# Kernel tuning notes

Hardware: AMD Instinct MI355X
Metric: run time of the kernel (lower is better)

Reference implementation:

```python
import jax, jax.numpy as jnp
import numpy as np

B, T, H, K = 128, 32, 256, 32


def setup_inputs() -> dict:
    key = jax.random.key(0)
    ks = jax.random.split(key, 24)
    s = 0.02  # small weight scale keeps exp(pdf) stable

    def n(k, shape, scale=s):
        return jax.random.normal(k, shape, dtype=jnp.float32) * scale

    inp = {
        "input_encoded": jax.random.normal(ks[0], (B, T, H), dtype=jnp.float32),
        "y_prev": jax.random.normal(ks[1], (B, T), dtype=jnp.float32),
        "attn_W1": n(ks[2], (H, 3 * H)),
        "attn_b1": n(ks[3], (H,)),
        "attn_W2": n(ks[4], (1, H)),
        "attn_b2": n(ks[5], (1,)),
        "fc_W": n(ks[6], (1, H + 1)),
        "fc_b": n(ks[7], (1,)),
        "var_W": n(ks[8], (H, H + 1)),
        "var_b": n(ks[9], (H,)),
        "W_ih": n(ks[10], (4 * H, 1)),
        "W_hh": n(ks[11], (4 * H, H)),
        "b_ih": n(ks[12], (4 * H,)),
        "b_hh": n(ks[13], (4 * H,)),
        "fc_dec_W": n(ks[14], (1, H)),
        "fc_dec_b": n(ks[15], (1,)),
        "pdf_W": n(ks[16], (1, H + 1)),
        "pdf_b": n(ks[17], (1,)),
        "fc_enc_W": n(ks[18], (1, H)),
        "fc_enc_b": n(ks[19], (1,)),
        "num_particles": K,
    }
    return inp


def reference(input_encoded, y_prev, attn_W1, attn_b1, attn_W2, attn_b2,
              fc_W, fc_b, var_W, var_b, W_ih, W_hh, b_ih, b_hh,
              fc_dec_W, fc_dec_b, pdf_W, pdf_b, fc_enc_W, fc_enc_b,
              num_particles):
    Bn, Tn, Hn = input_encoded.shape
    Kn = num_particles
    base = jax.random.key(42)
    arB = jnp.arange(Bn)

    def step(carry, xs):
        hiddens, cells = carry  # each (K*B, H), flat index = k*B + b
        t, y_t = xs  # y_t: (B,)
        k1, k2 = jax.random.split(jax.random.fold_in(base, t))
        # particle means (torch: mean over dim 0 of (K, B, H) view)
        hm = hiddens.reshape(Kn, Bn, Hn).mean(axis=0)  # (B, H)
        cm = cells.reshape(Kn, Bn, Hn).mean(axis=0)
        # attention over encoder timesteps
        x = jnp.concatenate([
            jnp.broadcast_to(hm[:, None, :], (Bn, Tn, Hn)),
            jnp.broadcast_to(cm[:, None, :], (Bn, Tn, Hn)),
            input_encoded], axis=2)  # (B, T, 3H)
        a = jnp.tanh(x @ attn_W1.T + attn_b1) @ attn_W2.T + attn_b2  # (B, T, 1)
        beta = jax.nn.softmax(a[..., 0], axis=1)  # (B, T)
        context = jnp.einsum('bt,bth->bh', beta, input_encoded)  # (B, H)
        y_tilde = jnp.concatenate([context, y_t[:, None]], axis=1) @ fc_W.T + fc_b  # (B, 1)
        var = jnp.concatenate([y_tilde, hm], axis=1) @ var_W.T + var_b  # (B, H)
        # single-step LSTM cell over all particles (torch gate order i,f,g,o)
        x_in = jnp.tile(y_tilde, (Kn, 1))  # (K*B, 1)
        gates = x_in @ W_ih.T + b_ih + hiddens @ W_hh.T + b_hh  # (K*B, 4H)
        i, f, g, o = jnp.split(gates, 4, axis=1)
        c_new = jax.nn.sigmoid(f) * cells + jax.nn.sigmoid(i) * jnp.tanh(g)
        h_new = jax.nn.sigmoid(o) * jnp.tanh(c_new)
        # reparameterization: h = mu + eps * softplus(var)
        std = jnp.tile(jax.nn.softplus(var), (Kn, 1))  # (K*B, H)
        eps = jax.random.normal(k1, (Kn * Bn, Hn), dtype=h_new.dtype)
        h_new = h_new + eps * std
        # sort_hidden: per-batch argsort of 1-d projection, gather hiddens only
        proj = h_new @ fc_dec_W.T + fc_dec_b  # (K*B, 1)
        idx = jnp.argsort(proj.reshape(Kn, Bn).T, axis=1)  # (B, K)
        flat = (arB[:, None] + idx * Bn).T.reshape(-1)  # (K*B,)
        h_sorted = h_new[flat]
        # particle weights (replicates torch's view(-1, K, 1) reshape exactly)
        y = jnp.concatenate([h_sorted, jnp.tile(y_tilde, (Kn, 1))], axis=1)
        prob = jnp.exp(y @ pdf_W.T + pdf_b).reshape(Bn, Kn, 1)
        prob = prob / prob.sum(axis=1, keepdims=True)
        # soft-resampling: multinomial over (B, K) rows (torch: prob.view(K,-1).T)
        logits = jnp.log(prob.reshape(Kn, Bn).T)  # (B, K)
        samp = jax.random.categorical(k2, logits, shape=(Kn, Bn))  # (K, B)
        flat2 = (samp * Bn + arB[None, :]).reshape(-1)
        return (h_sorted[flat2], c_new[flat2]), context

    h0 = jnp.zeros((Kn * Bn, Hn), dtype=input_encoded.dtype)
    (hiddens, _), contexts = jax.lax.scan(step, (h0, h0), (jnp.arange(Tn), y_prev.T))
    context = contexts[-1]
    hm = hiddens.reshape(Kn, Bn, Hn).mean(axis=0)  # (B, H)
    y_pred = hm @ fc_dec_W.T + fc_dec_b + context @ fc_enc_W.T + fc_enc_b  # (B, 1)
    return y_pred
```

## Files before the change

kernel.cpp:

```cpp
#include <hip/hip_runtime.h>
#include <cstdint>


#define Bn 128
#define Tn 32
#define Hn 256
#define Kn 32

__host__ __device__ inline void tf2x32(uint32_t k0, uint32_t k1, uint32_t x0, uint32_t x1,
                                       uint32_t &o0, uint32_t &o1) {
  uint32_t ks2 = k0 ^ k1 ^ 0x1BD11BDAu;
  x0 += k0; x1 += k1;
#define TFR(r) { x0 += x1; x1 = (x1 << r) | (x1 >> (32 - r)); x1 ^= x0; }
  TFR(13) TFR(15) TFR(26) TFR(6)
  x0 += k1;  x1 += ks2 + 1u;
  TFR(17) TFR(29) TFR(16) TFR(24)
  x0 += ks2; x1 += k0 + 2u;
  TFR(13) TFR(15) TFR(26) TFR(6)
  x0 += k0;  x1 += k1 + 3u;
  TFR(17) TFR(29) TFR(16) TFR(24)
  x0 += k1;  x1 += ks2 + 4u;
  TFR(13) TFR(15) TFR(26) TFR(6)
  x0 += ks2; x1 += k0 + 5u;
#undef TFR
  o0 = x0; o1 = x1;
}

__device__ __forceinline__ float erfinv_xla(float x) {
  float w = -log1pf(-x * x);
  float p;
  if (w < 5.0f) {
    w = w - 2.5f;
    p = 2.81022636e-08f;
    p = fmaf(p, w, 3.43273939e-07f);
    p = fmaf(p, w, -3.5233877e-06f);
    p = fmaf(p, w, -4.39150654e-06f);
    p = fmaf(p, w, 0.00021858087f);
    p = fmaf(p, w, -0.00125372503f);
    p = fmaf(p, w, -0.00417768164f);
    p = fmaf(p, w, 0.246640727f);
    p = fmaf(p, w, 1.50140941f);
  } else {
    w = sqrtf(w) - 3.0f;
    p = -0.000200214257f;
    p = fmaf(p, w, 0.000100950558f);
    p = fmaf(p, w, 0.00134934322f);
    p = fmaf(p, w, -0.00367342844f);
    p = fmaf(p, w, 0.00573950773f);
    p = fmaf(p, w, -0.0076224613f);
    p = fmaf(p, w, 0.00943887047f);
    p = fmaf(p, w, 1.00167406f);
    p = fmaf(p, w, 2.83297682f);
  }
  return p * x;
}

__device__ __forceinline__ float sigmoid_xla(float x) {
  return 0.5f + 0.5f * tanhf(0.5f * x);
}

__device__ __forceinline__ float u01_from_bits(uint32_t bits) {
  return __uint_as_float((bits >> 9) | 0x3F800000u) - 1.0f;
}

__device__ __forceinline__ float normal_from_idx(uint32_t ka, uint32_t kb, uint32_t idx) {
  uint32_t o0, o1; tf2x32(ka, kb, 0u, idx, o0, o1);
  float f = u01_from_bits(o0 ^ o1);
  const float LO = __uint_as_float(0xBF7FFFFFu);
  float u = fmaxf(LO, f * 2.0f + LO);
  return __uint_as_float(0x3FB504F3u) * erfinv_xla(u);
}

__device__ __forceinline__ float gumbel_from_idx(uint32_t ka, uint32_t kb, uint32_t idx) {
  uint32_t o0, o1; tf2x32(ka, kb, 0u, idx, o0, o1);
  float f = u01_from_bits(o0 ^ o1);
  const float TINY = __uint_as_float(0x00800000u);
  float u = fmaxf(TINY, f + TINY);
  return -logf(-logf(u));
}


__global__ void darnn_p0(const float* __restrict__ W1, const float* __restrict__ Whh,
                         const float* __restrict__ varW,
                         float* __restrict__ W1hT, float* __restrict__ W1cT,
                         float* __restrict__ W1eT, float* __restrict__ WhhT,
                         float* __restrict__ varWT) {
  int bid = blockIdx.x, tid = threadIdx.x;
  if (bid < 768) {
    int part = bid >> 8, j = bid & 255;
    float v = W1[tid * 768 + part * 256 + j];
    float* dst = (part == 0) ? W1hT : (part == 1) ? W1cT : W1eT;
    dst[j * 256 + tid] = v;
  } else if (bid < 1024) {
    int j = bid - 768;
    for (int idx = tid; idx < 1024; idx += 256) {
      int h = idx >> 2, q = idx & 3;
      WhhT[j * 1024 + idx] = Whh[(q * 256 + h) * 256 + j];
    }
  } else {
    int j2 = bid - 1024;
    varWT[j2 * 256 + tid] = varW[tid * 257 + j2];
  }
}

__global__ void darnn_p1(const float* __restrict__ enc, const float* __restrict__ W1eT,
                         const float* __restrict__ b1, float* __restrict__ encW1) {
  int bt = blockIdx.x, tid = threadIdx.x;
  __shared__ float se[256];
  se[tid] = enc[bt * 256 + tid];
  __syncthreads();
  float acc = 0.f;
  for (int j = 0; j < 256; ++j) acc = fmaf(se[j], W1eT[j * 256 + tid], acc);
  encW1[bt * 256 + tid] = acc + b1[tid];
}


__launch_bounds__(1024)
__global__ void darnn_ka(const float* __restrict__ enc, const float* __restrict__ yprev,
                         const float* __restrict__ W1hT, const float* __restrict__ W1cT,
                         const float* __restrict__ encW1, const float* __restrict__ W2,
                         const float* __restrict__ b2p, const float* __restrict__ fcW,
                         const float* __restrict__ fcbp, const float* __restrict__ varWT,
                         const float* __restrict__ varb, const float* __restrict__ pdfW,
                         const float* __restrict__ pdfbp,
                         const float* __restrict__ proj_g, const float* __restrict__ pdot_g,
                         const float* __restrict__ ytl_prev,
                         const float* __restrict__ hprev, const float* __restrict__ cprev,
                         int* __restrict__ idxH_g, int* __restrict__ idxC_g,
                         float* __restrict__ ytl_cur, float* __restrict__ std_g,
                         float* __restrict__ ctx_g,
                         int t, uint32_t k2a, uint32_t k2b) {
  const int b = blockIdx.x, tid = threadIdx.x, bg = b >> 5, bloc = b & 31;
  __shared__ float s_gp[1024], s_w[1024];
  __shared__ int s_srck[1024];
  __shared__ float s_ytlp[32], s_den[32], s_logit[32];
  __shared__ int s_row[32], s_rowc[32];
  __shared__ float s_hm[256], s_cm[256], s_hmc[256], s_red[256];
  __shared__ float s_sc[32], s_beta[32];
  __shared__ float s_ytl;

  if (t > 0) {
    if (tid < 32) s_ytlp[tid] = ytl_prev[bg * 32 + tid];
    {
      int bl = tid >> 5, k = tid & 31;
      s_gp[tid] = proj_g[k * 128 + bg * 32 + bl];
    }
    __syncthreads();
    {
      int bl = tid >> 5, k = tid & 31;
      float p = s_gp[tid];
      const float* gp = s_gp + bl * 32;
      int rank = 0;
      for (int kk = 0; kk < 32; ++kk) {
        float q = gp[kk];
        rank += (q < p) || (q == p && kk < k);
      }
      s_srck[bl * 32 + rank] = k;
      float wv = expf((pdot_g[k * 128 + bg * 32 + bl] + s_ytlp[bl] * pdfW[256]) + pdfbp[0]);
      s_w[bl * 32 + rank] = wv;
    }
    __syncthreads();
    if (tid < 32) {
      float s = 0.f;
      for (int bl = 0; bl < 32; ++bl) s += s_w[bl * 32 + tid];
      s_den[tid] = s;
    }
    __syncthreads();
    if (tid < 32) s_logit[tid] = logf(s_w[bloc * 32 + tid] / s_den[tid]);
    __syncthreads();
    if (tid < 32) {
      int ko = tid, r2 = ko * 128 + b;
      float best = gumbel_from_idx(k2a, k2b, (uint32_t)(r2 * 32)) + s_logit[0];
      int sv = 0;
      for (int k = 1; k < 32; ++k) {
        float v = gumbel_from_idx(k2a, k2b, (uint32_t)(r2 * 32 + k)) + s_logit[k];
        if (v > best) { best = v; sv = k; }
      }
      int sH = s_srck[bloc * 32 + sv];
      s_row[ko] = sH * 128 + b;
      s_rowc[ko] = sv * 128 + b;
      idxH_g[ko * 128 + b] = sH * 128 + b;
      idxC_g[ko * 128 + b] = sv * 128 + b;
    }
  } else {
    if (tid < 32) {
      s_row[tid] = tid * 128 + b;
      s_rowc[tid] = tid * 128 + b;
      idxH_g[tid * 128 + b] = tid * 128 + b;
      idxC_g[tid * 128 + b] = tid * 128 + b;
    }
  }
  __syncthreads();

  if (tid < 256) {
    float s1 = 0.f;
    for (int k = 0; k < 32; ++k) s1 += hprev[(size_t)s_row[k] * 256 + tid];
    s_hm[tid] = s1 * 0.03125f;
  } else if (tid < 512) {
    int j = tid & 255;
    float s2 = 0.f;
    for (int k = 0; k < 32; ++k) s2 += cprev[(size_t)s_rowc[k] * 256 + j];
    s_cm[j] = s2 * 0.03125f;
  }
  __syncthreads();
  if (tid < 256) {
    float acc = 0.f;
    for (int j = 0; j < 256; ++j) {
      acc = fmaf(s_hm[j], W1hT[j * 256 + tid], acc);
      acc = fmaf(s_cm[j], W1cT[j * 256 + tid], acc);
    }
    s_hmc[tid] = acc;
  }
  __syncthreads();
  {
    int lane = tid & 63, wv = tid >> 6;
    for (int tt = wv * 2; tt < wv * 2 + 2; ++tt) {
      float p = 0.f;
      for (int hh = lane; hh < 256; hh += 64)
        p += tanhf(encW1[(b * 32 + tt) * 256 + hh] + s_hmc[hh]) * W2[hh];
      for (int off = 32; off; off >>= 1) p += __shfl_down(p, off);
      if (lane == 0) s_sc[tt] = p + b2p[0];
    }
  }
  __syncthreads();
  if (tid == 0) {
    float m = s_sc[0];
    for (int k = 1; k < 32; ++k) m = fmaxf(m, s_sc[k]);
    float s = 0.f;
    for (int k = 0; k < 32; ++k) { float e = expf(s_sc[k] - m); s_beta[k] = e; s += e; }
    for (int k = 0; k < 32; ++k) s_beta[k] /= s;
  }
  __syncthreads();
  if (tid < 256) {
    float cx = 0.f;
    for (int tt = 0; tt < 32; ++tt) cx = fmaf(s_beta[tt], enc[(b * 32 + tt) * 256 + tid], cx);
    ctx_g[b * 256 + tid] = cx;
    s_red[tid] = cx * fcW[tid];
  }
  __syncthreads();
  if (tid == 0) {
    float s = 0.f;
    for (int j = 0; j < 256; ++j) s += s_red[j];
    s += yprev[b * 32 + t] * fcW[256];
    s_ytl = s + fcbp[0];
    ytl_cur[b] = s_ytl;
  }
  __syncthreads();
  if (tid < 256) {
    float v = s_ytl * varWT[tid];
    for (int j = 0; j < 256; ++j) v = fmaf(s_hm[j], varWT[(1 + j) * 256 + tid], v);
    v += varb[tid];
    std_g[b * 256 + tid] = fmaxf(v, 0.f) + log1pf(expf(-fabsf(v)));
  }
}


__launch_bounds__(1024)
__global__ void darnn_k5(const float* __restrict__ hprev, const float* __restrict__ cprev,
                         const int* __restrict__ idxH_g, const int* __restrict__ idxC_g,
                         const float* __restrict__ WhhT, const float* __restrict__ Wih,
                         const float* __restrict__ bih, const float* __restrict__ bhh,
                         const float* __restrict__ ytl_cur, const float* __restrict__ std_g,
                         const float* __restrict__ decW, const float* __restrict__ decbp,
                         const float* __restrict__ pdfW,
                         uint32_t k1a, uint32_t k1b,
                         float* __restrict__ hcur, float* __restrict__ ccur,
                         float* __restrict__ proj_g, float* __restrict__ pdot_g) {
  const int R0 = blockIdx.x * 16, tid = threadIdx.x;
  const int h = tid & 255, kg = tid >> 8, lane = tid & 63;
  __shared__ __align__(16) float s_h[16 * 256];
  __shared__ int s_src[16], s_srcC[16];
  __shared__ float s_sredP[16 * 4], s_sredQ[16 * 4];

  if (tid < 16) { s_src[tid] = idxH_g[R0 + tid]; s_srcC[tid] = idxC_g[R0 + tid]; }
  __syncthreads();
  {
    const float4* hp = (const float4*)hprev;
    float4* sh4 = (float4*)s_h;
    int rr = tid >> 6, c4 = tid & 63;
    sh4[tid] = hp[(size_t)s_src[rr] * 64 + c4];
  }
  __syncthreads();

  float ai[4], af[4], ag[4], ao[4];
#pragma unroll
  for (int r = 0; r < 4; ++r) { ai[r] = af[r] = ag[r] = ao[r] = 0.f; }
  {
    const float4* wp = (const float4*)WhhT + h;
    const float* shr = s_h + kg * 4 * 256;
    for (int j = 0; j < 256; j += 4) {
      float4 w0 = wp[(j + 0) * 256];
      float4 w1 = wp[(j + 1) * 256];
      float4 w2 = wp[(j + 2) * 256];
      float4 w3 = wp[(j + 3) * 256];
#pragma unroll
      for (int r = 0; r < 4; ++r) {
        float4 h4 = *(const float4*)(shr + r * 256 + j);
        ai[r] = fmaf(h4.x, w0.x, ai[r]); ai[r] = fmaf(h4.y, w1.x, ai[r]);
        ai[r] = fmaf(h4.z, w2.x, ai[r]); ai[r] = fmaf(h4.w, w3.x, ai[r]);
        af[r] = fmaf(h4.x, w0.y, af[r]); af[r] = fmaf(h4.y, w1.y, af[r]);
        af[r] = fmaf(h4.z, w2.y, af[r]); af[r] = fmaf(h4.w, w3.y, af[r]);
        ag[r] = fmaf(h4.x, w0.z, ag[r]); ag[r] = fmaf(h4.y, w1.z, ag[r]);
        ag[r] = fmaf(h4.z, w2.z, ag[r]); ag[r] = fmaf(h4.w, w3.z, ag[r]);
        ao[r] = fmaf(h4.x, w0.w, ao[r]); ao[r] = fmaf(h4.y, w1.w, ao[r]);
        ao[r] = fmaf(h4.z, w2.w, ao[r]); ao[r] = fmaf(h4.w, w3.w, ao[r]);
      }
    }
  }

  const float bI = bih[h], bF = bih[256 + h], bG = bih[512 + h], bO = bih[768 + h];
  const float dI = bhh[h], dF = bhh[256 + h], dG = bhh[512 + h], dO = bhh[768 + h];
  const float wI = Wih[h], wF = Wih[256 + h], wG = Wih[512 + h], wO = Wih[768 + h];
  float hnv[4];
#pragma unroll
  for (int r = 0; r < 4; ++r) {
    int rr = kg * 4 + r, R = R0 + rr, bb = R & 127;
    float xb = ytl_cur[bb];
    float pi = ((xb * wI + bI) + ai[r]) + dI;
    float pf = ((xb * wF + bF) + af[r]) + dF;
    float pg = ((xb * wG + bG) + ag[r]) + dG;
    float po = ((xb * wO + bO) + ao[r]) + dO;
    float c_old = cprev[(size_t)s_srcC[rr] * 256 + h];
    float cn = sigmoid_xla(pf) * c_old + sigmoid_xla(pi) * tanhf(pg);
    float hn = sigmoid_xla(po) * tanhf(cn);
    float eps = normal_from_idx(k1a, k1b, (uint32_t)(R * 256 + h));
    hn = hn + eps * std_g[bb * 256 + h];
    ccur[(size_t)R * 256 + h] = cn;
    hcur[(size_t)R * 256 + h] = hn;
    hnv[r] = hn;
  }

  const float dw = decW[h], pw = pdfW[h];
#pragma unroll
  for (int r = 0; r < 4; ++r) {
    int rr = kg * 4 + r;
    float v = hnv[r] * dw;
    for (int off = 32; off; off >>= 1) v += __shfl_down(v, off);
    if (lane == 0) s_sredP[rr * 4 + (h >> 6)] = v;
    float v2 = hnv[r] * pw;
    for (int off = 32; off; off >>= 1) v2 += __shfl_down(v2, off);
    if (lane == 0) s_sredQ[rr * 4 + (h >> 6)] = v2;
  }
  __syncthreads();
  if (tid < 16) {
    int rr = tid;
    proj_g[R0 + rr] = ((s_sredP[rr * 4 + 0] + s_sredP[rr * 4 + 1]) +
                       (s_sredP[rr * 4 + 2] + s_sredP[rr * 4 + 3])) + decbp[0];
  } else if (tid < 32) {
    int rr = tid - 16;
    pdot_g[R0 + rr] = (s_sredQ[rr * 4 + 0] + s_sredQ[rr * 4 + 1]) +
                      (s_sredQ[rr * 4 + 2] + s_sredQ[rr * 4 + 3]);
  }
}


__launch_bounds__(256)
__global__ void darnn_kout(const float* __restrict__ proj_g, const float* __restrict__ pdot_g,
                           const float* __restrict__ ytl_prev, const float* __restrict__ hprev,
                           const float* __restrict__ ctx_g, const float* __restrict__ decW,
                           const float* __restrict__ decbp, const float* __restrict__ encWo,
                           const float* __restrict__ encbo, const float* __restrict__ pdfW,
                           const float* __restrict__ pdfbp,
                           uint32_t k2a, uint32_t k2b, float* __restrict__ out) {
  const int b = blockIdx.x, tid = threadIdx.x, bg = b >> 5, bloc = b & 31;
  const int lane = tid & 63;
  __shared__ float s_gp[1024], s_w[1024];
  __shared__ int s_srck[1024];
  __shared__ float s_ytlp[32], s_den[32], s_logit[32];
  __shared__ int s_row[32];
  __shared__ float s_hm[256], s_sred[8];

  if (tid < 32) s_ytlp[tid] = ytl_prev[bg * 32 + tid];
  for (int i = tid; i < 1024; i += 256) {
    int bl = i >> 5, k = i & 31;
    s_gp[i] = proj_g[k * 128 + bg * 32 + bl];
  }
  __syncthreads();
  for (int i = tid; i < 1024; i += 256) {
    int bl = i >> 5, k = i & 31;
    float p = s_gp[i];
    const float* gp = s_gp + bl * 32;
    int rank = 0;
    for (int kk = 0; kk < 32; ++kk) {
      float q = gp[kk];
      rank += (q < p) || (q == p && kk < k);
    }
    s_srck[bl * 32 + rank] = k;
    float wv = expf((pdot_g[k * 128 + bg * 32 + bl] + s_ytlp[bl] * pdfW[256]) + pdfbp[0]);
    s_w[bl * 32 + rank] = wv;
  }
  __syncthreads();
  if (tid < 32) {
    float s = 0.f;
    for (int bl = 0; bl < 32; ++bl) s += s_w[bl * 32 + tid];
    s_den[tid] = s;
  }
  __syncthreads();
  if (tid < 32) s_logit[tid] = logf(s_w[bloc * 32 + tid] / s_den[tid]);
  __syncthreads();
  if (tid < 32) {
    int ko = tid, r2 = ko * 128 + b;
    float best = gumbel_from_idx(k2a, k2b, (uint32_t)(r2 * 32)) + s_logit[0];
    int sv = 0;
    for (int k = 1; k < 32; ++k) {
      float v = gumbel_from_idx(k2a, k2b, (uint32_t)(r2 * 32 + k)) + s_logit[k];
      if (v > best) { best = v; sv = k; }
    }
    s_row[ko] = s_srck[bloc * 32 + sv] * 128 + b;
  }
  __syncthreads();
  {
    float s1 = 0.f;
    for (int k = 0; k < 32; ++k) s1 += hprev[(size_t)s_row[k] * 256 + tid];
    s_hm[tid] = s1 * 0.03125f;
  }
  __syncthreads();
  {
    int wvi = tid >> 6;
    float v1 = s_hm[tid] * decW[tid];
    float v2 = ctx_g[b * 256 + tid] * encWo[tid];
    for (int off = 32; off; off >>= 1) { v1 += __shfl_down(v1, off); v2 += __shfl_down(v2, off); }
    if (lane == 0) { s_sred[wvi] = v1; s_sred[4 + wvi] = v2; }
  }
  __syncthreads();
  if (tid == 0) {
    float d1 = (s_sred[0] + s_sred[1]) + (s_sred[2] + s_sred[3]);
    float d2 = (s_sred[4] + s_sred[5]) + (s_sred[6] + s_sred[7]);
    out[b] = ((d1 + decbp[0]) + d2) + encbo[0];
  }
}

extern "C" void kernel_launch(void* const* d_in, const int* in_sizes, int n_in,
                              void* d_out, int out_size, void* d_ws, size_t ws_size,
                              hipStream_t stream) {
  const float* enc   = (const float*)d_in[0];
  const float* yprev = (const float*)d_in[1];
  const float* W1    = (const float*)d_in[2];
  const float* b1    = (const float*)d_in[3];
  const float* W2    = (const float*)d_in[4];
  const float* b2    = (const float*)d_in[5];
  const float* fcW   = (const float*)d_in[6];
  const float* fcb   = (const float*)d_in[7];
  const float* varW  = (const float*)d_in[8];
  const float* varb  = (const float*)d_in[9];
  const float* Wih   = (const float*)d_in[10];
  const float* Whh   = (const float*)d_in[11];
  const float* bih   = (const float*)d_in[12];
  const float* bhh   = (const float*)d_in[13];
  const float* decW  = (const float*)d_in[14];
  const float* decb  = (const float*)d_in[15];
  const float* pdfW  = (const float*)d_in[16];
  const float* pdfb  = (const float*)d_in[17];
  const float* encWo = (const float*)d_in[18];
  const float* encbo = (const float*)d_in[19];

  float* ws = (float*)d_ws;
  size_t o = 0;
  float* encW1 = ws + o; o += (size_t)Bn * Tn * Hn;
  float* W1hT  = ws + o; o += (size_t)Hn * Hn;
  float* W1cT  = ws + o; o += (size_t)Hn * Hn;
  float* W1eT  = ws + o; o += (size_t)Hn * Hn;
  float* WhhT  = ws + o; o += (size_t)Hn * 4 * Hn;
  float* varWT = ws + o; o += (size_t)257 * Hn;
  float* hbuf0 = ws + o; o += (size_t)Kn * Bn * Hn;
  float* hbuf1 = ws + o; o += (size_t)Kn * Bn * Hn;
  float* cbuf0 = ws + o; o += (size_t)Kn * Bn * Hn;
  float* cbuf1 = ws + o; o += (size_t)Kn * Bn * Hn;
  float* ytl0  = ws + o; o += 128;
  float* ytl1  = ws + o; o += 128;
  float* std_g = ws + o; o += (size_t)Bn * Hn;
  float* ctx_g = ws + o; o += (size_t)Bn * Hn;
  float* proj_g = ws + o; o += 4096;
  float* pdot_g = ws + o; o += 4096;
  int*   idxH  = (int*)(ws + o); o += 4096;
  int*   idxC  = (int*)(ws + o); o += 4096;
  if (ws_size < o * sizeof(float)) return;

  float* hb[2] = { hbuf0, hbuf1 };
  float* cb[2] = { cbuf0, cbuf1 };
  float* yb[2] = { ytl0, ytl1 };

  hipMemsetAsync(hbuf1, 0, (size_t)Kn * Bn * Hn * sizeof(float), stream);
  hipMemsetAsync(cbuf1, 0, (size_t)Kn * Bn * Hn * sizeof(float), stream);

  darnn_p0<<<1281, 256, 0, stream>>>(W1, Whh, varW, W1hT, W1cT, W1eT, WhhT, varWT);
  darnn_p1<<<Bn * Tn, 256, 0, stream>>>(enc, W1eT, b1, encW1);

  uint32_t k2pa = 0, k2pb = 0;
  for (int t = 0; t < Tn; ++t) {
    uint32_t f0, f1, k1a, k1b, k2a, k2b;
    tf2x32(0u, 42u, 0u, (uint32_t)t, f0, f1);
    tf2x32(f0, f1, 0u, 0u, k1a, k1b);
    tf2x32(f0, f1, 0u, 1u, k2a, k2b);
    int cur = t & 1, prv = (t + 1) & 1;

    darnn_ka<<<Bn, 1024, 0, stream>>>(enc, yprev, W1hT, W1cT, encW1, W2, b2, fcW, fcb,
                                      varWT, varb, pdfW, pdfb,
                                      proj_g, pdot_g, yb[prv], hb[prv], cb[prv],
                                      idxH, idxC, yb[cur], std_g, ctx_g,
                                      t, k2pa, k2pb);
    darnn_k5<<<Kn * Bn / 16, 1024, 0, stream>>>(hb[prv], cb[prv], idxH, idxC, WhhT,
                                                Wih, bih, bhh, yb[cur], std_g,
                                                decW, decb, pdfW, k1a, k1b,
                                                hb[cur], cb[cur], proj_g, pdot_g);
    k2pa = k2a; k2pb = k2b;
  }

  darnn_kout<<<Bn, 256, 0, stream>>>(proj_g, pdot_g, yb[1], hb[1], ctx_g,
                                     decW, decb, encWo, encbo, pdfW, pdfb,
                                     k2pa, k2pb, (float*)d_out);
}
```

Before: 3.010 ms.

## Fuse attention and LSTM step kernels into one per-timestep kernel

Merges the per-step attention/resampling kernel and the LSTM particle-update kernel into a single kernel launched with two blocks per batch element, each handling half of the particles. Resampling indices, std, and ytl now stay in shared memory instead of passing through global buffers, and proj/pdot outputs are double-buffered so a step can read the previous values while writing new ones. The attention part (mean, W1 projection, softmax, context, var projection) is recomputed redundantly by both blocks of a batch. The Whh loop also adds software prefetching of the next weight rows into registers. The cost is larger shared memory per block and higher register pressure, which may reduce occupancy.

```diff
diff --git a/kernel.cpp b/kernel.cpp
--- a/kernel.cpp
+++ b/kernel.cpp
@@ -115,35 +115,44 @@
 }
 
 
-__launch_bounds__(1024)
-__global__ void darnn_ka(const float* __restrict__ enc, const float* __restrict__ yprev,
-                         const float* __restrict__ W1hT, const float* __restrict__ W1cT,
-                         const float* __restrict__ encW1, const float* __restrict__ W2,
-                         const float* __restrict__ b2p, const float* __restrict__ fcW,
-                         const float* __restrict__ fcbp, const float* __restrict__ varWT,
-                         const float* __restrict__ varb, const float* __restrict__ pdfW,
-                         const float* __restrict__ pdfbp,
-                         const float* __restrict__ proj_g, const float* __restrict__ pdot_g,
-                         const float* __restrict__ ytl_prev,
-                         const float* __restrict__ hprev, const float* __restrict__ cprev,
-                         int* __restrict__ idxH_g, int* __restrict__ idxC_g,
-                         float* __restrict__ ytl_cur, float* __restrict__ std_g,
-                         float* __restrict__ ctx_g,
-                         int t, uint32_t k2a, uint32_t k2b) {
-  const int b = blockIdx.x, tid = threadIdx.x, bg = b >> 5, bloc = b & 31;
+__launch_bounds__(1024, 4)
+__global__ void darnn_step(const float* __restrict__ enc, const float* __restrict__ yprev,
+                           const float* __restrict__ W1hT, const float* __restrict__ W1cT,
+                           const float* __restrict__ encW1, const float* __restrict__ W2,
+                           const float* __restrict__ b2p, const float* __restrict__ fcW,
+                           const float* __restrict__ fcbp, const float* __restrict__ varWT,
+                           const float* __restrict__ varb, const float* __restrict__ WhhT,
+                           const float* __restrict__ Wih, const float* __restrict__ bih,
+                           const float* __restrict__ bhh, const float* __restrict__ decW,
+                           const float* __restrict__ decbp, const float* __restrict__ pdfW,
+                           const float* __restrict__ pdfbp,
+                           const float* __restrict__ proj_p, const float* __restrict__ pdot_p,
+                           const float* __restrict__ ytl_p,
+                           const float* __restrict__ hprev, const float* __restrict__ cprev,
+                           float* __restrict__ hcur, float* __restrict__ ccur,
+                           float* __restrict__ proj_c, float* __restrict__ pdot_c,
+                           float* __restrict__ ytl_c, float* __restrict__ ctx_g,
+                           int t, uint32_t k1a, uint32_t k1b, uint32_t k2a, uint32_t k2b) {
+  const int bid = blockIdx.x, tid = threadIdx.x;
+  const int b = bid & 127, khalf = bid >> 7;
+  const int bg = b >> 5, bloc = b & 31;
+  const int h = tid & 255, kg = tid >> 8, lane = tid & 63;
+
+  __shared__ __align__(16) float s_h[32 * 256];
   __shared__ float s_gp[1024], s_w[1024];
   __shared__ int s_srck[1024];
   __shared__ float s_ytlp[32], s_den[32], s_logit[32];
-  __shared__ int s_row[32], s_rowc[32];
-  __shared__ float s_hm[256], s_cm[256], s_hmc[256], s_red[256];
+  __shared__ int s_rowH[32], s_rowC[32];
+  __shared__ float s_hm[256], s_cm[256], s_hmc[256], s_red[256], s_std[256];
   __shared__ float s_sc[32], s_beta[32];
   __shared__ float s_ytl;
+  __shared__ float s_sredP[16 * 4], s_sredQ[16 * 4];
 
   if (t > 0) {
-    if (tid < 32) s_ytlp[tid] = ytl_prev[bg * 32 + tid];
+    if (tid < 32) s_ytlp[tid] = ytl_p[bg * 32 + tid];
     {
       int bl = tid >> 5, k = tid & 31;
-      s_gp[tid] = proj_g[k * 128 + bg * 32 + bl];
+      s_gp[tid] = proj_p[k * 128 + bg * 32 + bl];
     }
     __syncthreads();
     {
@@ -156,7 +165,7 @@
         rank += (q < p) || (q == p && kk < k);
       }
       s_srck[bl * 32 + rank] = k;
-      float wv = expf((pdot_g[k * 128 + bg * 32 + bl] + s_ytlp[bl] * pdfW[256]) + pdfbp[0]);
+      float wv = expf((pdot_p[k * 128 + bg * 32 + bl] + s_ytlp[bl] * pdfW[256]) + pdfbp[0]);
       s_w[bl * 32 + rank] = wv;
     }
     __syncthreads();
@@ -176,30 +185,37 @@
         float v = gumbel_from_idx(k2a, k2b, (uint32_t)(r2 * 32 + k)) + s_logit[k];
         if (v > best) { best = v; sv = k; }
       }
-      int sH = s_srck[bloc * 32 + sv];
-      s_row[ko] = sH * 128 + b;
-      s_rowc[ko] = sv * 128 + b;
-      idxH_g[ko * 128 + b] = sH * 128 + b;
-      idxC_g[ko * 128 + b] = sv * 128 + b;
+      s_rowH[ko] = s_srck[bloc * 32 + sv] * 128 + b;
+      s_rowC[ko] = sv * 128 + b;
     }
   } else {
     if (tid < 32) {
-      s_row[tid] = tid * 128 + b;
-      s_rowc[tid] = tid * 128 + b;
-      idxH_g[tid * 128 + b] = tid * 128 + b;
-      idxC_g[tid * 128 + b] = tid * 128 + b;
+      s_rowH[tid] = tid * 128 + b;
+      s_rowC[tid] = tid * 128 + b;
+    }
+  }
+  __syncthreads();
+
+  {
+    const float4* hp = (const float4*)hprev;
+    float4* sh4 = (float4*)s_h;
+#pragma unroll
+    for (int ii = 0; ii < 2; ++ii) {
+      int i = tid + ii * 1024;
+      int rr = i >> 6, c4 = i & 63;
+      sh4[i] = hp[(size_t)s_rowH[rr] * 64 + c4];
     }
   }
   __syncthreads();
 
   if (tid < 256) {
     float s1 = 0.f;
-    for (int k = 0; k < 32; ++k) s1 += hprev[(size_t)s_row[k] * 256 + tid];
+    for (int k = 0; k < 32; ++k) s1 += s_h[k * 256 + tid];
     s_hm[tid] = s1 * 0.03125f;
   } else if (tid < 512) {
     int j = tid & 255;
     float s2 = 0.f;
-    for (int k = 0; k < 32; ++k) s2 += cprev[(size_t)s_rowc[k] * 256 + j];
+    for (int k = 0; k < 32; ++k) s2 += cprev[(size_t)s_rowC[k] * 256 + j];
     s_cm[j] = s2 * 0.03125f;
   }
   __syncthreads();
@@ -213,7 +229,7 @@
   }
   __syncthreads();
   {
-    int lane = tid & 63, wv = tid >> 6;
+    int wv = tid >> 6;
     for (int tt = wv * 2; tt < wv * 2 + 2; ++tt) {
       float p = 0.f;
       for (int hh = lane; hh < 256; hh += 64)
@@ -234,7 +250,7 @@
   if (tid < 256) {
     float cx = 0.f;
     for (int tt = 0; tt < 32; ++tt) cx = fmaf(s_beta[tt], enc[(b * 32 + tt) * 256 + tid], cx);
-    ctx_g[b * 256 + tid] = cx;
+    if (khalf == 0) ctx_g[b * 256 + tid] = cx;
     s_red[tid] = cx * fcW[tid];
   }
   __syncthreads();
@@ -243,42 +259,14 @@
     for (int j = 0; j < 256; ++j) s += s_red[j];
     s += yprev[b * 32 + t] * fcW[256];
     s_ytl = s + fcbp[0];
-    ytl_cur[b] = s_ytl;
+    if (khalf == 0) ytl_c[b] = s_ytl;
   }
   __syncthreads();
   if (tid < 256) {
     float v = s_ytl * varWT[tid];
     for (int j = 0; j < 256; ++j) v = fmaf(s_hm[j], varWT[(1 + j) * 256 + tid], v);
     v += varb[tid];
-    std_g[b * 256 + tid] = fmaxf(v, 0.f) + log1pf(expf(-fabsf(v)));
-  }
-}
-
-
-__launch_bounds__(1024)
-__global__ void darnn_k5(const float* __restrict__ hprev, const float* __restrict__ cprev,
-                         const int* __restrict__ idxH_g, const int* __restrict__ idxC_g,
-                         const float* __restrict__ WhhT, const float* __restrict__ Wih,
-                         const float* __restrict__ bih, const float* __restrict__ bhh,
-                         const float* __restrict__ ytl_cur, const float* __restrict__ std_g,
-                         const float* __restrict__ decW, const float* __restrict__ decbp,
-                         const float* __restrict__ pdfW,
-                         uint32_t k1a, uint32_t k1b,
-                         float* __restrict__ hcur, float* __restrict__ ccur,
-                         float* __restrict__ proj_g, float* __restrict__ pdot_g) {
-  const int R0 = blockIdx.x * 16, tid = threadIdx.x;
-  const int h = tid & 255, kg = tid >> 8, lane = tid & 63;
-  __shared__ __align__(16) float s_h[16 * 256];
-  __shared__ int s_src[16], s_srcC[16];
-  __shared__ float s_sredP[16 * 4], s_sredQ[16 * 4];
-
-  if (tid < 16) { s_src[tid] = idxH_g[R0 + tid]; s_srcC[tid] = idxC_g[R0 + tid]; }
-  __syncthreads();
-  {
-    const float4* hp = (const float4*)hprev;
-    float4* sh4 = (float4*)s_h;
-    int rr = tid >> 6, c4 = tid & 63;
-    sh4[tid] = hp[(size_t)s_src[rr] * 64 + c4];
+    s_std[tid] = fmaxf(v, 0.f) + log1pf(expf(-fabsf(v)));
   }
   __syncthreads();
 
@@ -287,24 +275,27 @@
   for (int r = 0; r < 4; ++r) { ai[r] = af[r] = ag[r] = ao[r] = 0.f; }
   {
     const float4* wp = (const float4*)WhhT + h;
-    const float* shr = s_h + kg * 4 * 256;
+    const float* shr = s_h + (khalf * 16 + kg * 4) * 256;
+    float4 wa0 = wp[0 * 256], wa1 = wp[1 * 256], wa2 = wp[2 * 256], wa3 = wp[3 * 256];
     for (int j = 0; j < 256; j += 4) {
-      float4 w0 = wp[(j + 0) * 256];
-      float4 w1 = wp[(j + 1) * 256];
-      float4 w2 = wp[(j + 2) * 256];
-      float4 w3 = wp[(j + 3) * 256];
+      int jn = (j + 4) & 255;
+      float4 wb0 = wp[(jn + 0) * 256];
+      float4 wb1 = wp[(jn + 1) * 256];
+      float4 wb2 = wp[(jn + 2) * 256];
+      float4 wb3 = wp[(jn + 3) * 256];
 #pragma unroll
       for (int r = 0; r < 4; ++r) {
         float4 h4 = *(const float4*)(shr + r * 256 + j);
-        ai[r] = fmaf(h4.x, w0.x, ai[r]); ai[r] = fmaf(h4.y, w1.x, ai[r]);
-        ai[r] = fmaf(h4.z, w2.x, ai[r]); ai[r] = fmaf(h4.w, w3.x, ai[r]);
-        af[r] = fmaf(h4.x, w0.y, af[r]); af[r] = fmaf(h4.y, w1.y, af[r]);
-        af[r] = fmaf(h4.z, w2.y, af[r]); af[r] = fmaf(h4.w, w3.y, af[r]);
-        ag[r] = fmaf(h4.x, w0.z, ag[r]); ag[r] = fmaf(h4.y, w1.z, ag[r]);
-        ag[r] = fmaf(h4.z, w2.z, ag[r]); ag[r] = fmaf(h4.w, w3.z, ag[r]);
-        ao[r] = fmaf(h4.x, w0.w, ao[r]); ao[r] = fmaf(h4.y, w1.w, ao[r]);
-        ao[r] = fmaf(h4.z, w2.w, ao[r]); ao[r] = fmaf(h4.w, w3.w, ao[r]);
+        ai[r] = fmaf(h4.x, wa0.x, ai[r]); ai[r] = fmaf(h4.y, wa1.x, ai[r]);
+        ai[r] = fmaf(h4.z, wa2.x, ai[r]); ai[r] = fmaf(h4.w, wa3.x, ai[r]);
+        af[r] = fmaf(h4.x, wa0.y, af[r]); af[r] = fmaf(h4.y, wa1.y, af[r]);
+        af[r] = fmaf(h4.z, wa2.y, af[r]); af[r] = fmaf(h4.w, wa3.y, af[r]);
+        ag[r] = fmaf(h4.x, wa0.z, ag[r]); ag[r] = fmaf(h4.y, wa1.z, ag[r]);
+        ag[r] = fmaf(h4.z, wa2.z, ag[r]); ag[r] = fmaf(h4.w, wa3.z, ag[r]);
+        ao[r] = fmaf(h4.x, wa0.w, ao[r]); ao[r] = fmaf(h4.y, wa1.w, ao[r]);
+        ao[r] = fmaf(h4.z, wa2.w, ao[r]); ao[r] = fmaf(h4.w, wa3.w, ao[r]);
       }
+      wa0 = wb0; wa1 = wb1; wa2 = wb2; wa3 = wb3;
     }
   }
 
@@ -314,17 +305,18 @@
   float hnv[4];
 #pragma unroll
   for (int r = 0; r < 4; ++r) {
-    int rr = kg * 4 + r, R = R0 + rr, bb = R & 127;
-    float xb = ytl_cur[bb];
+    int rl = kg * 4 + r;
+    int k = khalf * 16 + rl, R = k * 128 + b;
+    float xb = s_ytl;
     float pi = ((xb * wI + bI) + ai[r]) + dI;
     float pf = ((xb * wF + bF) + af[r]) + dF;
     float pg = ((xb * wG + bG) + ag[r]) + dG;
     float po = ((xb * wO + bO) + ao[r]) + dO;
-    float c_old = cprev[(size_t)s_srcC[rr] * 256 + h];
+    float c_old = cprev[(size_t)s_rowC[k] * 256 + h];
     float cn = sigmoid_xla(pf) * c_old + sigmoid_xla(pi) * tanhf(pg);
     float hn = sigmoid_xla(po) * tanhf(cn);
     float eps = normal_from_idx(k1a, k1b, (uint32_t)(R * 256 + h));
-    hn = hn + eps * std_g[bb * 256 + h];
+    hn = hn + eps * s_std[h];
     ccur[(size_t)R * 256 + h] = cn;
     hcur[(size_t)R * 256 + h] = hn;
     hnv[r] = hn;
@@ -333,23 +325,23 @@
   const float dw = decW[h], pw = pdfW[h];
 #pragma unroll
   for (int r = 0; r < 4; ++r) {
-    int rr = kg * 4 + r;
+    int rl = kg * 4 + r;
     float v = hnv[r] * dw;
     for (int off = 32; off; off >>= 1) v += __shfl_down(v, off);
-    if (lane == 0) s_sredP[rr * 4 + (h >> 6)] = v;
+    if (lane == 0) s_sredP[rl * 4 + (h >> 6)] = v;
     float v2 = hnv[r] * pw;
     for (int off = 32; off; off >>= 1) v2 += __shfl_down(v2, off);
-    if (lane == 0) s_sredQ[rr * 4 + (h >> 6)] = v2;
+    if (lane == 0) s_sredQ[rl * 4 + (h >> 6)] = v2;
   }
   __syncthreads();
   if (tid < 16) {
-    int rr = tid;
-    proj_g[R0 + rr] = ((s_sredP[rr * 4 + 0] + s_sredP[rr * 4 + 1]) +
-                       (s_sredP[rr * 4 + 2] + s_sredP[rr * 4 + 3])) + decbp[0];
+    int rl = tid, k = khalf * 16 + rl;
+    proj_c[k * 128 + b] = ((s_sredP[rl * 4 + 0] + s_sredP[rl * 4 + 1]) +
+                           (s_sredP[rl * 4 + 2] + s_sredP[rl * 4 + 3])) + decbp[0];
   } else if (tid < 32) {
-    int rr = tid - 16;
-    pdot_g[R0 + rr] = (s_sredQ[rr * 4 + 0] + s_sredQ[rr * 4 + 1]) +
-                      (s_sredQ[rr * 4 + 2] + s_sredQ[rr * 4 + 3]);
+    int rl = tid - 16, k = khalf * 16 + rl;
+    pdot_c[k * 128 + b] = (s_sredQ[rl * 4 + 0] + s_sredQ[rl * 4 + 1]) +
+                          (s_sredQ[rl * 4 + 2] + s_sredQ[rl * 4 + 3]);
   }
 }
 
@@ -468,17 +460,18 @@
   float* cbuf1 = ws + o; o += (size_t)Kn * Bn * Hn;
   float* ytl0  = ws + o; o += 128;
   float* ytl1  = ws + o; o += 128;
-  float* std_g = ws + o; o += (size_t)Bn * Hn;
   float* ctx_g = ws + o; o += (size_t)Bn * Hn;
-  float* proj_g = ws + o; o += 4096;
-  float* pdot_g = ws + o; o += 4096;
-  int*   idxH  = (int*)(ws + o); o += 4096;
-  int*   idxC  = (int*)(ws + o); o += 4096;
+  float* proj0 = ws + o; o += 4096;
+  float* proj1 = ws + o; o += 4096;
+  float* pdot0 = ws + o; o += 4096;
+  float* pdot1 = ws + o; o += 4096;
   if (ws_size < o * sizeof(float)) return;
 
   float* hb[2] = { hbuf0, hbuf1 };
   float* cb[2] = { cbuf0, cbuf1 };
   float* yb[2] = { ytl0, ytl1 };
+  float* pp[2] = { proj0, proj1 };
+  float* pq[2] = { pdot0, pdot1 };
 
   hipMemsetAsync(hbuf1, 0, (size_t)Kn * Bn * Hn * sizeof(float), stream);
   hipMemsetAsync(cbuf1, 0, (size_t)Kn * Bn * Hn * sizeof(float), stream);
@@ -494,19 +487,16 @@
     tf2x32(f0, f1, 0u, 1u, k2a, k2b);
     int cur = t & 1, prv = (t + 1) & 1;
 
-    darnn_ka<<<Bn, 1024, 0, stream>>>(enc, yprev, W1hT, W1cT, encW1, W2, b2, fcW, fcb,
-                                      varWT, varb, pdfW, pdfb,
-                                      proj_g, pdot_g, yb[prv], hb[prv], cb[prv],
-                                      idxH, idxC, yb[cur], std_g, ctx_g,
-                                      t, k2pa, k2pb);
-    darnn_k5<<<Kn * Bn / 16, 1024, 0, stream>>>(hb[prv], cb[prv], idxH, idxC, WhhT,
-                                                Wih, bih, bhh, yb[cur], std_g,
-                                                decW, decb, pdfW, k1a, k1b,
-                                                hb[cur], cb[cur], proj_g, pdot_g);
+    darnn_step<<<2 * Bn, 1024, 0, stream>>>(enc, yprev, W1hT, W1cT, encW1, W2, b2,
+                                            fcW, fcb, varWT, varb, WhhT, Wih, bih, bhh,
+                                            decW, decb, pdfW, pdfb,
+                                            pp[prv], pq[prv], yb[prv], hb[prv], cb[prv],
+                                            hb[cur], cb[cur], pp[cur], pq[cur], yb[cur],
+                                            ctx_g, t, k1a, k1b, k2pa, k2pb);
     k2pa = k2a; k2pb = k2b;
   }
 
-  darnn_kout<<<Bn, 256, 0, stream>>>(proj_g, pdot_g, yb[1], hb[1], ctx_g,
+  darnn_kout<<<Bn, 256, 0, stream>>>(pp[1], pq[1], yb[1], hb[1], ctx_g,
                                      decW, decb, encWo, encbo, pdfW, pdfb,
                                      k2pa, k2pb, (float*)d_out);
 }
```

Result: faster. 2.866 ms (-4.8%).
